# Kernel optimization log

Hardware: AMD Instinct MI355X
Metric: run time of the kernel (lower is better)

Reference implementation:

```python
import jax, jax.numpy as jnp
import numpy as np
import math

D_MODEL = 512
N_HEADS = 8
MAX_SPAN = 512
SPAN_LOSS_COEF = 2e-4
NEG_INF = -1.0e9
R_SIZE = 4.0


def soft_span_mask(span, max_span, seq_len):
    # span: (H,) clamped span fractions
    i_idx = jnp.arange(seq_len, dtype=span.dtype)[:, None]
    j_idx = jnp.arange(seq_len, dtype=span.dtype)[None, :]
    dist = i_idx - j_idx                                  # (T, T)
    eff_span = (span * max_span)[:, None, None]           # (H, 1, 1)
    x = eff_span - dist[None, :, :]                       # (H, T, T)
    R = jnp.clip((x + 1.0) / R_SIZE, 0.0, 1.0)
    causal_ok = dist[None, :, :] >= 0
    log_R = jnp.maximum(jnp.log(R + 1e-10), NEG_INF)
    return jnp.where(causal_ok & (R > 0), log_R, NEG_INF)  # (H, T, T)


def setup_inputs() -> dict:
    key = jax.random.key(0)
    ks = jax.random.split(key, 6)
    B, T, D = 4, 2048, D_MODEL
    w_scale = 0.02
    return {
        "x": jax.random.normal(ks[0], (B, T, D), dtype=jnp.float32),
        "wq": jax.random.normal(ks[1], (D, D), dtype=jnp.float32) * w_scale,
        "wk": jax.random.normal(ks[2], (D, D), dtype=jnp.float32) * w_scale,
        "wv": jax.random.normal(ks[3], (D, D), dtype=jnp.float32) * w_scale,
        "wo": jax.random.normal(ks[4], (D, D), dtype=jnp.float32) * w_scale,
        "span_params": jax.random.uniform(ks[5], (N_HEADS,), dtype=jnp.float32),
    }


def reference(x, wq, wk, wv, wo, span_params):
    B, T, D = x.shape
    H = N_HEADS
    d_h = D // H

    clamped_span = jnp.clip(span_params, 0.0, 1.0)

    # nn.Linear(bias=False): y = x @ W.T
    Q = (x @ wq.T).reshape(B, T, H, d_h).transpose(0, 2, 1, 3)  # (B,H,T,dh)
    K = (x @ wk.T).reshape(B, T, H, d_h).transpose(0, 2, 1, 3)
    V = (x @ wv.T).reshape(B, T, H, d_h).transpose(0, 2, 1, 3)

    scale = 1.0 / math.sqrt(d_h)
    scores = jnp.einsum("bhqd,bhkd->bhqk", Q, K) * scale        # (B,H,T,T)
    scores = scores + soft_span_mask(clamped_span, MAX_SPAN, T)[None]

    weights = jax.nn.softmax(scores, axis=-1)
    out = jnp.einsum("bhqk,bhkd->bhqd", weights, V)             # (B,H,T,dh)
    out = out.transpose(0, 2, 1, 3).reshape(B, T, D)
    output = out @ wo.T

    span_loss = SPAN_LOSS_COEF * clamped_span.mean()
    return output, span_loss
```

## Files before the change

kernel.cpp:

```cpp
#include <hip/hip_runtime.h>
#include <math.h>

#define T_SEQ   2048
#define DMODEL  512
#define NHEADS  8
#define DH      64
#define NEG_INF -1.0e9f

typedef __attribute__((ext_vector_type(8))) short short8;
typedef __attribute__((ext_vector_type(4))) float f32x4;
typedef unsigned int u32;
typedef unsigned short u16;

__device__ __forceinline__ u16 f2bf(float f) {
    union { float f; u32 u; } w; w.f = f;
    return (u16)((w.u + 0x8000u) >> 16);
}

__device__ __forceinline__ void async_load16(const u16* g, u16* l) {
    __builtin_amdgcn_global_load_lds(
        (const __attribute__((address_space(1))) u32*)(const void*)g,
        (__attribute__((address_space(3))) u32*)(void*)l, 16, 0, 0);
}

__global__ void cast_all(const float* __restrict__ x,  const float* __restrict__ wq,
                         const float* __restrict__ wk, const float* __restrict__ wv,
                         const float* __restrict__ wo, const float* __restrict__ sp,
                         u16* __restrict__ xb,  u16* __restrict__ wqb,
                         u16* __restrict__ wkb, u16* __restrict__ wvb,
                         u16* __restrict__ wob, float* __restrict__ loss_out)
{
    const int bid = blockIdx.x;
    const float* src; u16* dst; int i;
    if (bid < 4096) { src = x; dst = xb; i = bid * 256 + threadIdx.x; }
    else {
        const int wsel = (bid - 4096) >> 8;
        src = (wsel == 0) ? wq : (wsel == 1) ? wk : (wsel == 2) ? wv : wo;
        dst = (wsel == 0) ? wqb : (wsel == 1) ? wkb : (wsel == 2) ? wvb : wob;
        i = ((bid - 4096) & 255) * 256 + threadIdx.x;
    }
    float4 v = ((const float4*)src)[i];
    ushort4 o;
    o.x = f2bf(v.x); o.y = f2bf(v.y); o.z = f2bf(v.z); o.w = f2bf(v.w);
    ((ushort4*)dst)[i] = o;
    if (bid == 5119 && threadIdx.x == 0) {
        float s = 0.0f;
        for (int h = 0; h < NHEADS; ++h)
            s += fminf(fmaxf(sp[h], 0.0f), 1.0f);
        loss_out[0] = 2e-4f * (s * 0.125f);
    }
}

__global__ __launch_bounds__(256)
void gemm_bf16(const u16* __restrict__ A,
               const u16* __restrict__ W0, const u16* __restrict__ W1,
               const u16* __restrict__ W2,
               u16* __restrict__ Cb0, u16* __restrict__ Cb1,
               u16* __restrict__ Cb2,
               float* __restrict__ Cf, int scatter)
{
    constexpr int K = 512, BK = 64;
    const u16* W  = (blockIdx.z == 0) ? W0 : (blockIdx.z == 1) ? W1 : W2;
    u16*       Cb = (blockIdx.z == 0) ? Cb0 : (blockIdx.z == 1) ? Cb1 : Cb2;

    __shared__ __align__(16) u16 smem[16384];
    u16* As = smem;
    u16* Bs = smem + 8192;

    const int t    = threadIdx.x;
    const int lane = t & 63;
    const int wave = t >> 6;
    const int wm   = wave >> 1, wn = wave & 1;
    const int m0   = blockIdx.x * 128, n0 = blockIdx.y * 128;

    const int srow = t >> 3;
    const int kb   = (t & 7) ^ (srow & 7);
    const u16* gA = A + (size_t)(m0 + srow) * K + kb * 8;
    const u16* gW = W + (size_t)(n0 + srow) * K + kb * 8;

    const int rA = wm * 64 + (lane & 15);
    const int rB = wn * 64 + (lane & 15);
    const int kq = lane >> 4;
    const int offA0 = rA * BK + ((kq      ^ (rA & 7)) * 8);
    const int offA1 = rA * BK + (((4 + kq) ^ (rA & 7)) * 8);
    const int offB0 = rB * BK + ((kq      ^ (rB & 7)) * 8);
    const int offB1 = rB * BK + (((4 + kq) ^ (rB & 7)) * 8);

    f32x4 acc[4][4];
#pragma unroll
    for (int it = 0; it < 4; ++it)
#pragma unroll
        for (int jt = 0; jt < 4; ++jt) acc[it][jt] = (f32x4)0.0f;

    for (int k0 = 0; k0 < K; k0 += BK) {
        __syncthreads();
#pragma unroll
        for (int i = 0; i < 4; ++i) {
            async_load16(gA + k0 + i * (32 * K), As + t * 8 + i * 2048);
            async_load16(gW + k0 + i * (32 * K), Bs + t * 8 + i * 2048);
        }
        __syncthreads();

        short8 af[4][2], bfr[4][2];
#pragma unroll
        for (int it = 0; it < 4; ++it) {
            af[it][0]  = *(const short8*)(As + offA0 + it * 16 * BK);
            af[it][1]  = *(const short8*)(As + offA1 + it * 16 * BK);
            bfr[it][0] = *(const short8*)(Bs + offB0 + it * 16 * BK);
            bfr[it][1] = *(const short8*)(Bs + offB1 + it * 16 * BK);
        }
#pragma unroll
        for (int it = 0; it < 4; ++it)
#pragma unroll
            for (int jt = 0; jt < 4; ++jt) {
                acc[it][jt] = __builtin_amdgcn_mfma_f32_16x16x32_bf16(
                    af[it][0], bfr[jt][0], acc[it][jt], 0, 0, 0);
                acc[it][jt] = __builtin_amdgcn_mfma_f32_16x16x32_bf16(
                    af[it][1], bfr[jt][1], acc[it][jt], 0, 0, 0);
            }
    }

    const int r0 = (lane >> 4) * 4;
    const int cl = lane & 15;

    if (scatter) {
        constexpr int P = 136;
#pragma unroll
        for (int rnd = 0; rnd < 2; ++rnd) {
            __syncthreads();
#pragma unroll
            for (int s = 0; s < 2; ++s) {
                const int it = rnd * 2 + s;
                const int lrow = wm * 32 + s * 16 + r0;
#pragma unroll
                for (int jt = 0; jt < 4; ++jt) {
                    const int cc = wn * 64 + jt * 16 + cl;
#pragma unroll
                    for (int r = 0; r < 4; ++r)
                        smem[(lrow + r) * P + cc] = f2bf(acc[it][jt][r]);
                }
            }
            __syncthreads();
            const int lrow2 = t >> 2;
            const int h2    = (t >> 1) & 1;
            const int dhalf = t & 1;
            const int grow  = m0 + (lrow2 >> 5) * 64 + rnd * 32 + (lrow2 & 31);
            const int b     = grow >> 11, tt = grow & 2047;
            const int h     = (n0 >> 6) + h2;
            u16* dst = Cb + ((size_t)((b * NHEADS + h) * T_SEQ + tt)) * DH + dhalf * 32;
            const u16* srcl = smem + lrow2 * P + h2 * 64 + dhalf * 32;
#pragma unroll
            for (int i = 0; i < 4; ++i)
                ((uint4*)dst)[i] = *(const uint4*)(srcl + i * 8);
        }
    } else {
#pragma unroll
        for (int it = 0; it < 4; ++it) {
#pragma unroll
            for (int r = 0; r < 4; ++r) {
                const int row = m0 + wm * 64 + it * 16 + r0 + r;
#pragma unroll
                for (int jt = 0; jt < 4; ++jt) {
                    const int col = n0 + wn * 64 + jt * 16 + cl;
                    Cf[(size_t)row * DMODEL + col] = acc[it][jt][r];
                }
            }
        }
    }
}

__global__ __launch_bounds__(256)
void transpose_v(const u16* __restrict__ V, u16* __restrict__ Vt)
{
    __shared__ u16 tile[64][72];
    const int bh = blockIdx.y;
    const int j0 = blockIdx.x * 64;
    const u16* src = V + (size_t)bh * (T_SEQ * DH) + (size_t)j0 * DH;
    u16* dst = Vt + (size_t)bh * (T_SEQ * DH) + j0;
    const int t = threadIdx.x;
    const int jr = t >> 2, c0 = (t & 3) * 16;
    uint4 a = *(const uint4*)(src + (size_t)jr * DH + c0);
    uint4 b = *(const uint4*)(src + (size_t)jr * DH + c0 + 8);
    *(uint4*)&tile[jr][c0]     = a;
    *(uint4*)&tile[jr][c0 + 8] = b;
    __syncthreads();
    const int d = t >> 2, jc = (t & 3) * 16;
    union { uint4 v; u16 s[8]; } pa, pb;
#pragma unroll
    for (int i = 0; i < 8; ++i) pa.s[i] = tile[jc + i][d];
#pragma unroll
    for (int i = 0; i < 8; ++i) pb.s[i] = tile[jc + 8 + i][d];
    *(uint4*)(dst + (size_t)d * T_SEQ + jc)     = pa.v;
    *(uint4*)(dst + (size_t)d * T_SEQ + jc + 8) = pb.v;
}

__global__ __launch_bounds__(128)
void attn_mfma(const u16* __restrict__ Q, const u16* __restrict__ K,
               const u16* __restrict__ Vt, const float* __restrict__ span_params,
               u16* __restrict__ out)
{
    __shared__ __align__(16) u16 Ks[64 * 64];
    __shared__ __align__(16) u16 Vs[64 * 64];
    __shared__ __align__(16) u16 Ps[2][16 * 76];

    const int tid  = threadIdx.x;
    const int lane = tid & 63;
    const int w    = tid >> 6;
    const int nl   = lane & 15;
    const int quad = lane >> 4;

    const int l  = blockIdx.x;
    const int h  = l >> 8;
    const int b  = (l >> 6) & 3;
    const int qb = l & 63;
    const int bh = b * 8 + h;
    const int i0 = qb * 32;
    const int q0 = i0 + w * 16;

    const u16* Qh = Q  + (size_t)bh * (T_SEQ * DH);
    const u16* Kh = K  + (size_t)bh * (T_SEQ * DH);
    const u16* Vh = Vt + (size_t)bh * (DH * T_SEQ);

    float span = span_params[h];
    span = fminf(fmaxf(span, 0.0f), 1.0f);
    const float eff_span = span * 512.0f;
    const int wspan = (int)(eff_span + 1.0f) + 1;

    const float SCL = 0.125f * 1.44269504f;

    short8 qf0 = *(const short8*)(Qh + (size_t)(q0 + nl) * DH + quad * 8);
    short8 qf1 = *(const short8*)(Qh + (size_t)(q0 + nl) * DH + 32 + quad * 8);

    const int srow = tid >> 3;
    const int sg   = (tid & 7) ^ (srow & 7);
    const u16* gK = Kh + (size_t)srow * DH + sg * 8;
    const u16* gV = Vh + (size_t)srow * T_SEQ + sg * 8;

    f32x4 o[4];
    float m_r[4], l_r[4];
#pragma unroll
    for (int d = 0; d < 4; ++d) o[d] = (f32x4)0.0f;
#pragma unroll
    for (int r = 0; r < 4; ++r) { m_r[r] = -1.0e30f; l_r[r] = 0.0f; }

    int j_lo = i0 - wspan;
    if (j_lo < 0) j_lo = 0;
    j_lo &= ~63;

    for (int j0 = j_lo; j0 <= i0 + 31; j0 += 64) {
        __syncthreads();
#pragma unroll
        for (int i = 0; i < 4; ++i) {
            async_load16(gK + (size_t)(j0 + i * 16) * DH, Ks + tid * 8 + i * 1024);
            async_load16(gV + j0 + (size_t)(i * 16) * T_SEQ, Vs + tid * 8 + i * 1024);
        }
        __syncthreads();

        f32x4 s[4];
        bool any[4];
        __builtin_amdgcn_s_setprio(1);
#pragma unroll
        for (int n = 0; n < 4; ++n) {
            const int jn = j0 + n * 16;
            any[n] = (jn <= q0 + 15) &&
                     ((float)(q0 - jn - 15) < eff_span + 1.0f);
            s[n] = (f32x4)0.0f;
            if (any[n]) {
                const int row = n * 16 + nl;
                const u16* kp = Ks + row * 64;
                short8 b0 = *(const short8*)(kp + ((quad ^ (row & 7)) * 8));
                short8 b1 = *(const short8*)(kp + (((4 + quad) ^ (row & 7)) * 8));
                s[n] = __builtin_amdgcn_mfma_f32_16x16x32_bf16(qf0, b0, s[n], 0, 0, 0);
                s[n] = __builtin_amdgcn_mfma_f32_16x16x32_bf16(qf1, b1, s[n], 0, 0, 0);
            }
        }
        __builtin_amdgcn_s_setprio(0);

        float tmax[4] = {-1.0e30f, -1.0e30f, -1.0e30f, -1.0e30f};
#pragma unroll
        for (int n = 0; n < 4; ++n) {
            if (!any[n]) continue;
            const int jn = j0 + n * 16;
            const bool causal_b = (jn + 15 > q0);
            const bool span_b   = ((float)(q0 + 15 - jn) > eff_span - 3.0f);
            if (!causal_b && !span_b) {
#pragma unroll
                for (int r = 0; r < 4; ++r) {
                    const float sv = s[n][r] * SCL;
                    s[n][r] = sv;
                    tmax[r] = fmaxf(tmax[r], sv);
                }
            } else if (!span_b) {
#pragma unroll
                for (int r = 0; r < 4; ++r) {
                    const int dist = (q0 + quad * 4 + r) - (jn + nl);
                    const float sv = (dist >= 0) ? s[n][r] * SCL : NEG_INF;
                    s[n][r] = sv;
                    tmax[r] = fmaxf(tmax[r], sv);
                }
            } else {
#pragma unroll
                for (int r = 0; r < 4; ++r) {
                    const int dist = (q0 + quad * 4 + r) - (jn + nl);
                    float sv = NEG_INF;
                    if (dist >= 0) {
                        float xv = eff_span - (float)dist;
                        float R  = fminf(fmaxf((xv + 1.0f) * 0.25f, 0.0f), 1.0f);
                        if (R > 0.0f)
                            sv = s[n][r] * SCL +
                                 ((R < 1.0f) ? __log2f(R + 1e-10f) : 0.0f);
                    }
                    s[n][r] = sv;
                    tmax[r] = fmaxf(tmax[r], sv);
                }
            }
        }

        float alpha[4];
#pragma unroll
        for (int r = 0; r < 4; ++r) {
            float t2 = tmax[r];
            t2 = fmaxf(t2, __shfl_xor(t2, 1));
            t2 = fmaxf(t2, __shfl_xor(t2, 2));
            t2 = fmaxf(t2, __shfl_xor(t2, 4));
            t2 = fmaxf(t2, __shfl_xor(t2, 8));
            const float m_new = fmaxf(m_r[r], t2);
            alpha[r] = exp2f(m_r[r] - m_new);
            m_r[r] = m_new;
        }

        float psum[4] = {0.0f, 0.0f, 0.0f, 0.0f};
#pragma unroll
        for (int n = 0; n < 4; ++n) {
            if (any[n]) {
#pragma unroll
                for (int r = 0; r < 4; ++r) {
                    const float pv = exp2f(s[n][r] - m_r[r]);
                    psum[r] += pv;
                    Ps[w][(quad * 4 + r) * 76 + n * 16 + nl] = f2bf(pv);
                }
            } else {
#pragma unroll
                for (int r = 0; r < 4; ++r)
                    Ps[w][(quad * 4 + r) * 76 + n * 16 + nl] = 0;
            }
        }
#pragma unroll
        for (int r = 0; r < 4; ++r) {
            float ps = psum[r];
            ps += __shfl_xor(ps, 1);
            ps += __shfl_xor(ps, 2);
            ps += __shfl_xor(ps, 4);
            ps += __shfl_xor(ps, 8);
            l_r[r] = l_r[r] * alpha[r] + ps;
#pragma unroll
            for (int d = 0; d < 4; ++d) o[d][r] *= alpha[r];
        }

        const bool kf0 = any[0] | any[1];
        const bool kf1 = any[2] | any[3];
        const u16* pb = Ps[w] + nl * 76;
        short8 a0 = *(const short8*)(pb + quad * 8);
        short8 a1 = *(const short8*)(pb + 32 + quad * 8);
        __builtin_amdgcn_s_setprio(1);
#pragma unroll
        for (int d = 0; d < 4; ++d) {
            const int vrow = d * 16 + nl;
            const u16* vp = Vs + vrow * 64;
            if (kf0) {
                short8 vb0 = *(const short8*)(vp + ((quad ^ (vrow & 7)) * 8));
                o[d] = __builtin_amdgcn_mfma_f32_16x16x32_bf16(a0, vb0, o[d], 0, 0, 0);
            }
            if (kf1) {
                short8 vb1 = *(const short8*)(vp + (((4 + quad) ^ (vrow & 7)) * 8));
                o[d] = __builtin_amdgcn_mfma_f32_16x16x32_bf16(a1, vb1, o[d], 0, 0, 0);
            }
        }
        __builtin_amdgcn_s_setprio(0);
    }

#pragma unroll
    for (int r = 0; r < 4; ++r) {
        const int qg = q0 + quad * 4 + r;
        const float inv_l = 1.0f / l_r[r];
        u16* op = out + (size_t)(b * T_SEQ + qg) * DMODEL + h * 64;
#pragma unroll
        for (int d = 0; d < 4; ++d)
            op[d * 16 + nl] = f2bf(o[d][r] * inv_l);
    }
}

extern "C" void kernel_launch(void* const* d_in, const int* in_sizes, int n_in,
                              void* d_out, int out_size, void* d_ws, size_t ws_size,
                              hipStream_t stream)
{
    (void)in_sizes; (void)n_in; (void)out_size; (void)ws_size;
    const float* x  = (const float*)d_in[0];
    const float* wq = (const float*)d_in[1];
    const float* wk = (const float*)d_in[2];
    const float* wv = (const float*)d_in[3];
    const float* wo = (const float*)d_in[4];
    const float* sp = (const float*)d_in[5];
    float* out = (float*)d_out;

    const size_t elems = (size_t)4 * T_SEQ * DMODEL;
    u16* xb  = (u16*)d_ws;
    u16* Qb  = xb  + elems;
    u16* Kb  = Qb  + elems;
    u16* Vb  = Kb  + elems;
    u16* Vtb = Vb  + elems;
    u16* Ab  = Vtb + elems;
    u16* wqb = Ab  + elems;
    u16* wkb = wqb + 262144;
    u16* wvb = wkb + 262144;
    u16* wob = wvb + 262144;

    cast_all<<<5120, 256, 0, stream>>>(x, wq, wk, wv, wo, sp,
                                       xb, wqb, wkb, wvb, wob, out + elems);
    gemm_bf16<<<dim3(64, 4, 3), 256, 0, stream>>>(
        xb, wqb, wkb, wvb, Qb, Kb, Vb, nullptr, 1);
    transpose_v<<<dim3(32, 32), 256, 0, stream>>>(Vb, Vtb);
    attn_mfma<<<dim3(2048), 128, 0, stream>>>(Qb, Kb, Vtb, sp, Ab);
    gemm_bf16<<<dim3(64, 4, 1), 256, 0, stream>>>(
        Ab, wob, wob, wob, nullptr, nullptr, nullptr, out, 0);
}
```

Before: 155.0 us.

## Double-buffer K/V tiles with async prefetch in span attention loop

The K and V shared-memory tiles become double buffers. The next tile's async global-to-LDS loads are issued before computing on the current one, with explicit vmcnt waits and raw barriers in place of syncthreads. This is meant to hide global load latency behind the QK and PV MFMA work. It doubles LDS use for K/V, which may reduce occupancy, and it depends on the vmcnt(8) count being correct, including any other outstanding loads.

After: 175.3 us. 1.13x slower.

```diff
diff --git a/kernel.cpp b/kernel.cpp
--- a/kernel.cpp
+++ b/kernel.cpp
@@ -21,6 +21,12 @@
     __builtin_amdgcn_global_load_lds(
         (const __attribute__((address_space(1))) u32*)(const void*)g,
         (__attribute__((address_space(3))) u32*)(void*)l, 16, 0, 0);
+}
+
+__device__ __forceinline__ void barrier_raw() {
+    __builtin_amdgcn_sched_barrier(0);
+    asm volatile("s_barrier" ::: "memory");
+    __builtin_amdgcn_sched_barrier(0);
 }
 
 __global__ void cast_all(const float* __restrict__ x,  const float* __restrict__ wq,
@@ -194,13 +200,23 @@
     *(uint4*)(dst + (size_t)d * T_SEQ + jc + 8) = pb.v;
 }
 
+__device__ __forceinline__ void stage_kv(const u16* gK, const u16* gV,
+                                         u16* Ksb, u16* Vsb, int tid, int jj)
+{
+#pragma unroll
+    for (int i = 0; i < 4; ++i) {
+        async_load16(gK + (size_t)(jj + i * 16) * DH,    Ksb + tid * 8 + i * 1024);
+        async_load16(gV + jj + (size_t)(i * 16) * T_SEQ, Vsb + tid * 8 + i * 1024);
+    }
+}
+
 __global__ __launch_bounds__(128)
 void attn_mfma(const u16* __restrict__ Q, const u16* __restrict__ K,
                const u16* __restrict__ Vt, const float* __restrict__ span_params,
                u16* __restrict__ out)
 {
-    __shared__ __align__(16) u16 Ks[64 * 64];
-    __shared__ __align__(16) u16 Vs[64 * 64];
+    __shared__ __align__(16) u16 Ks[2][64 * 64];
+    __shared__ __align__(16) u16 Vs[2][64 * 64];
     __shared__ __align__(16) u16 Ps[2][16 * 76];
 
     const int tid  = threadIdx.x;
@@ -246,15 +262,24 @@
     int j_lo = i0 - wspan;
     if (j_lo < 0) j_lo = 0;
     j_lo &= ~63;
-
-    for (int j0 = j_lo; j0 <= i0 + 31; j0 += 64) {
-        __syncthreads();
-#pragma unroll
-        for (int i = 0; i < 4; ++i) {
-            async_load16(gK + (size_t)(j0 + i * 16) * DH, Ks + tid * 8 + i * 1024);
-            async_load16(gV + j0 + (size_t)(i * 16) * T_SEQ, Vs + tid * 8 + i * 1024);
-        }
-        __syncthreads();
+    const int nt = ((i0 + 31 - j_lo) >> 6) + 1;
+
+    stage_kv(gK, gV, Ks[0], Vs[0], tid, j_lo);
+
+    for (int t = 0; t < nt; ++t) {
+        const int j0  = j_lo + (t << 6);
+        const int buf = t & 1;
+
+        if (t + 1 < nt) {
+            stage_kv(gK, gV, Ks[buf ^ 1], Vs[buf ^ 1], tid, j0 + 64);
+            asm volatile("s_waitcnt vmcnt(8)" ::: "memory");
+        } else {
+            asm volatile("s_waitcnt vmcnt(0)" ::: "memory");
+        }
+        barrier_raw();
+
+        const u16* Kb = Ks[buf];
+        const u16* Vb = Vs[buf];
 
         f32x4 s[4];
         bool any[4];
@@ -267,7 +292,7 @@
             s[n] = (f32x4)0.0f;
             if (any[n]) {
                 const int row = n * 16 + nl;
-                const u16* kp = Ks + row * 64;
+                const u16* kp = Kb + row * 64;
                 short8 b0 = *(const short8*)(kp + ((quad ^ (row & 7)) * 8));
                 short8 b1 = *(const short8*)(kp + (((4 + quad) ^ (row & 7)) * 8));
                 s[n] = __builtin_amdgcn_mfma_f32_16x16x32_bf16(qf0, b0, s[n], 0, 0, 0);
@@ -366,7 +391,7 @@
 #pragma unroll
         for (int d = 0; d < 4; ++d) {
             const int vrow = d * 16 + nl;
-            const u16* vp = Vs + vrow * 64;
+            const u16* vp = Vb + vrow * 64;
             if (kf0) {
                 short8 vb0 = *(const short8*)(vp + ((quad ^ (vrow & 7)) * 8));
                 o[d] = __builtin_amdgcn_mfma_f32_16x16x32_bf16(a0, vb0, o[d], 0, 0, 0);
@@ -377,6 +402,8 @@
             }
         }
         __builtin_amdgcn_s_setprio(0);
+
+        barrier_raw();
     }
 
 #pragma unroll
```

## Transpose attention MFMA operands so each lane owns one query row

Applied to the files above, without the earlier changes.

Swaps the A/B operands of both MFMAs so the score and output accumulators are transposed: each lane now holds four keys (or four head dims) for a single query row. Row max and sum reductions become two cross-quad shuffles on one scalar instead of four 4-step shuffles per lane. Probabilities are packed with hardware bf16 conversion and written to an XOR-swizzled shared buffer as 8-byte stores. The output is stored as packed 8-byte writes. This cuts shuffle, ALU and LDS store work in the softmax stage, and also switches bf16 rounding to the hardware conversion.

After: 152.5 us. No clear change (-1.6%).

```diff
diff --git a/kernel.cpp b/kernel.cpp
--- a/kernel.cpp
+++ b/kernel.cpp
@@ -15,6 +15,12 @@
 __device__ __forceinline__ u16 f2bf(float f) {
     union { float f; u32 u; } w; w.f = f;
     return (u16)((w.u + 0x8000u) >> 16);
+}
+
+__device__ __forceinline__ u32 cvt_pk_bf16(float lo, float hi) {
+    u32 r;
+    asm("v_cvt_pk_bf16_f32 %0, %1, %2" : "=v"(r) : "v"(lo), "v"(hi));
+    return r;
 }
 
 __device__ __forceinline__ void async_load16(const u16* g, u16* l) {
@@ -201,13 +207,14 @@
 {
     __shared__ __align__(16) u16 Ks[64 * 64];
     __shared__ __align__(16) u16 Vs[64 * 64];
-    __shared__ __align__(16) u16 Ps[2][16 * 76];
+    __shared__ __align__(16) u16 Ps[2][1024];
 
     const int tid  = threadIdx.x;
     const int lane = tid & 63;
     const int w    = tid >> 6;
     const int nl   = lane & 15;
     const int quad = lane >> 4;
+    const int swz  = (nl & 7) << 3;
 
     const int l  = blockIdx.x;
     const int h  = l >> 8;
@@ -237,15 +244,15 @@
     const u16* gV = Vh + (size_t)srow * T_SEQ + sg * 8;
 
     f32x4 o[4];
-    float m_r[4], l_r[4];
+    float m_r = -1.0e30f, l_r = 0.0f;
 #pragma unroll
     for (int d = 0; d < 4; ++d) o[d] = (f32x4)0.0f;
-#pragma unroll
-    for (int r = 0; r < 4; ++r) { m_r[r] = -1.0e30f; l_r[r] = 0.0f; }
 
     int j_lo = i0 - wspan;
     if (j_lo < 0) j_lo = 0;
     j_lo &= ~63;
+
+    u16* Psw = Ps[w];
 
     for (int j0 = j_lo; j0 <= i0 + 31; j0 += 64) {
         __syncthreads();
@@ -270,17 +277,19 @@
                 const u16* kp = Ks + row * 64;
                 short8 b0 = *(const short8*)(kp + ((quad ^ (row & 7)) * 8));
                 short8 b1 = *(const short8*)(kp + (((4 + quad) ^ (row & 7)) * 8));
-                s[n] = __builtin_amdgcn_mfma_f32_16x16x32_bf16(qf0, b0, s[n], 0, 0, 0);
-                s[n] = __builtin_amdgcn_mfma_f32_16x16x32_bf16(qf1, b1, s[n], 0, 0, 0);
+                s[n] = __builtin_amdgcn_mfma_f32_16x16x32_bf16(b0, qf0, s[n], 0, 0, 0);
+                s[n] = __builtin_amdgcn_mfma_f32_16x16x32_bf16(b1, qf1, s[n], 0, 0, 0);
             }
         }
         __builtin_amdgcn_s_setprio(0);
 
-        float tmax[4] = {-1.0e30f, -1.0e30f, -1.0e30f, -1.0e30f};
+        const int qg = q0 + nl;
+        float tmax = -1.0e30f;
 #pragma unroll
         for (int n = 0; n < 4; ++n) {
             if (!any[n]) continue;
             const int jn = j0 + n * 16;
+            const int jb = jn + quad * 4;
             const bool causal_b = (jn + 15 > q0);
             const bool span_b   = ((float)(q0 + 15 - jn) > eff_span - 3.0f);
             if (!causal_b && !span_b) {
@@ -288,20 +297,20 @@
                 for (int r = 0; r < 4; ++r) {
                     const float sv = s[n][r] * SCL;
                     s[n][r] = sv;
-                    tmax[r] = fmaxf(tmax[r], sv);
+                    tmax = fmaxf(tmax, sv);
                 }
             } else if (!span_b) {
 #pragma unroll
                 for (int r = 0; r < 4; ++r) {
-                    const int dist = (q0 + quad * 4 + r) - (jn + nl);
+                    const int dist = qg - (jb + r);
                     const float sv = (dist >= 0) ? s[n][r] * SCL : NEG_INF;
                     s[n][r] = sv;
-                    tmax[r] = fmaxf(tmax[r], sv);
+                    tmax = fmaxf(tmax, sv);
                 }
             } else {
 #pragma unroll
                 for (int r = 0; r < 4; ++r) {
-                    const int dist = (q0 + quad * 4 + r) - (jn + nl);
+                    const int dist = qg - (jb + r);
                     float sv = NEG_INF;
                     if (dist >= 0) {
                         float xv = eff_span - (float)dist;
@@ -311,57 +320,45 @@
                                  ((R < 1.0f) ? __log2f(R + 1e-10f) : 0.0f);
                     }
                     s[n][r] = sv;
-                    tmax[r] = fmaxf(tmax[r], sv);
+                    tmax = fmaxf(tmax, sv);
                 }
             }
         }
 
-        float alpha[4];
-#pragma unroll
-        for (int r = 0; r < 4; ++r) {
-            float t2 = tmax[r];
-            t2 = fmaxf(t2, __shfl_xor(t2, 1));
-            t2 = fmaxf(t2, __shfl_xor(t2, 2));
-            t2 = fmaxf(t2, __shfl_xor(t2, 4));
-            t2 = fmaxf(t2, __shfl_xor(t2, 8));
-            const float m_new = fmaxf(m_r[r], t2);
-            alpha[r] = exp2f(m_r[r] - m_new);
-            m_r[r] = m_new;
-        }
-
-        float psum[4] = {0.0f, 0.0f, 0.0f, 0.0f};
+        float t2 = fmaxf(tmax, __shfl_xor(tmax, 16));
+        t2 = fmaxf(t2, __shfl_xor(t2, 32));
+        const float m_new = fmaxf(m_r, t2);
+        const float alpha = exp2f(m_r - m_new);
+        m_r = m_new;
+
+        float psum = 0.0f;
 #pragma unroll
         for (int n = 0; n < 4; ++n) {
+            u32 w0 = 0, w1 = 0;
             if (any[n]) {
-#pragma unroll
-                for (int r = 0; r < 4; ++r) {
-                    const float pv = exp2f(s[n][r] - m_r[r]);
-                    psum[r] += pv;
-                    Ps[w][(quad * 4 + r) * 76 + n * 16 + nl] = f2bf(pv);
-                }
-            } else {
-#pragma unroll
-                for (int r = 0; r < 4; ++r)
-                    Ps[w][(quad * 4 + r) * 76 + n * 16 + nl] = 0;
-            }
-        }
-#pragma unroll
-        for (int r = 0; r < 4; ++r) {
-            float ps = psum[r];
-            ps += __shfl_xor(ps, 1);
-            ps += __shfl_xor(ps, 2);
-            ps += __shfl_xor(ps, 4);
-            ps += __shfl_xor(ps, 8);
-            l_r[r] = l_r[r] * alpha[r] + ps;
-#pragma unroll
-            for (int d = 0; d < 4; ++d) o[d][r] *= alpha[r];
-        }
+                const float p0 = exp2f(s[n][0] - m_r);
+                const float p1 = exp2f(s[n][1] - m_r);
+                const float p2 = exp2f(s[n][2] - m_r);
+                const float p3 = exp2f(s[n][3] - m_r);
+                psum += (p0 + p1) + (p2 + p3);
+                w0 = cvt_pk_bf16(p0, p1);
+                w1 = cvt_pk_bf16(p2, p3);
+            }
+            uint2 wv; wv.x = w0; wv.y = w1;
+            *(uint2*)&Psw[nl * 64 + ((n * 16 + quad * 4) ^ swz)] = wv;
+        }
+        float ps = psum + __shfl_xor(psum, 16);
+        ps += __shfl_xor(ps, 32);
+        l_r = l_r * alpha + ps;
+#pragma unroll
+        for (int d = 0; d < 4; ++d)
+#pragma unroll
+            for (int r = 0; r < 4; ++r) o[d][r] *= alpha;
 
         const bool kf0 = any[0] | any[1];
         const bool kf1 = any[2] | any[3];
-        const u16* pb = Ps[w] + nl * 76;
-        short8 a0 = *(const short8*)(pb + quad * 8);
-        short8 a1 = *(const short8*)(pb + 32 + quad * 8);
+        short8 pa0 = *(const short8*)&Psw[nl * 64 + ((quad * 8) ^ swz)];
+        short8 pa1 = *(const short8*)&Psw[nl * 64 + ((32 + quad * 8) ^ swz)];
         __builtin_amdgcn_s_setprio(1);
 #pragma unroll
         for (int d = 0; d < 4; ++d) {
@@ -369,24 +366,24 @@
             const u16* vp = Vs + vrow * 64;
             if (kf0) {
                 short8 vb0 = *(const short8*)(vp + ((quad ^ (vrow & 7)) * 8));
-                o[d] = __builtin_amdgcn_mfma_f32_16x16x32_bf16(a0, vb0, o[d], 0, 0, 0);
+                o[d] = __builtin_amdgcn_mfma_f32_16x16x32_bf16(vb0, pa0, o[d], 0, 0, 0);
             }
             if (kf1) {
                 short8 vb1 = *(const short8*)(vp + (((4 + quad) ^ (vrow & 7)) * 8));
-                o[d] = __builtin_amdgcn_mfma_f32_16x16x32_bf16(a1, vb1, o[d], 0, 0, 0);
+                o[d] = __builtin_amdgcn_mfma_f32_16x16x32_bf16(vb1, pa1, o[d], 0, 0, 0);
             }
         }
         __builtin_amdgcn_s_setprio(0);
     }
 
-#pragma unroll
-    for (int r = 0; r < 4; ++r) {
-        const int qg = q0 + quad * 4 + r;
-        const float inv_l = 1.0f / l_r[r];
-        u16* op = out + (size_t)(b * T_SEQ + qg) * DMODEL + h * 64;
-#pragma unroll
-        for (int d = 0; d < 4; ++d)
-            op[d * 16 + nl] = f2bf(o[d][r] * inv_l);
+    const float inv_l = 1.0f / l_r;
+    u16* op = out + (size_t)(b * T_SEQ + q0 + nl) * DMODEL + h * 64 + quad * 4;
+#pragma unroll
+    for (int d = 0; d < 4; ++d) {
+        uint2 wv;
+        wv.x = cvt_pk_bf16(o[d][0] * inv_l, o[d][1] * inv_l);
+        wv.y = cvt_pk_bf16(o[d][2] * inv_l, o[d][3] * inv_l);
+        *(uint2*)(op + d * 16) = wv;
     }
 }
 
```
